# Performance work log

Measured on AMD Instinct MI355X. Metric: run time of the kernel, lower is better.

Reference implementation:

```python
import jax, jax.numpy as jnp
import numpy as np

B, N_HIS, GRAPH_DIM, EMB, N_PRE = 32, 12, 307, 32, 12
DAY_STAMPS, WEEK_STATES = 288, 7
HID = EMB * N_PRE  # 384
STD, MEAN = 50.0, 60.0
LN_EPS = 1e-3  # keras LayerNormalization default epsilon


def setup_inputs() -> dict:
    key = jax.random.key(0)
    ks = jax.random.split(key, 32)
    gn = lambda k, shape, s: (jax.random.normal(k, shape, jnp.float32) * s)
    # inputs: [B, 1+n_his, 2+graph_dim]; row 0 carries (week, date) ids, rows 1: carry data
    x_data = gn(ks[0], (B, N_HIS, GRAPH_DIM), 1.0)
    week = jax.random.randint(ks[1], (B,), 0, WEEK_STATES)
    date = jax.random.randint(ks[2], (B,), 0, DAY_STAMPS)
    inputs = jnp.zeros((B, 1 + N_HIS, 2 + GRAPH_DIM), jnp.float32)
    inputs = inputs.at[:, 0, 0].set(week.astype(jnp.float32))
    inputs = inputs.at[:, 0, 1].set(date.astype(jnp.float32))
    inputs = inputs.at[:, 1:, 2:].set(x_data)
    d = {
        'inputs': inputs,
        'conv_w': gn(ks[3], (EMB,), 0.5),        # 1x1 Conv2D on 1 input channel
        'conv_b': gn(ks[4], (EMB,), 0.1),
        'dws': gn(ks[5], (DAY_STAMPS, N_HIS, EMB, EMB, N_HIS), (2.0 / (EMB * N_HIS)) ** 0.5),
        'dbs': gn(ks[6], (DAY_STAMPS, GRAPH_DIM, EMB, N_HIS), 0.02),
        'ln_gamma': jnp.ones((N_HIS,), jnp.float32),
        'ln_beta': jnp.zeros((N_HIS,), jnp.float32),
        'tge2tg': gn(ks[7], (GRAPH_DIM, EMB, GRAPH_DIM), (1.0 / (GRAPH_DIM * EMB)) ** 0.5),
        'gte2gt': gn(ks[8], (N_HIS, EMB, N_HIS), (1.0 / (N_HIS * EMB)) ** 0.5),
        'fully_w': gn(ks[9], (2 * N_HIS, N_PRE), (1.0 / (2 * N_HIS)) ** 0.5),
    }
    shapes = [(N_HIS, HID), (HID,), (HID, HID), (HID,), (HID, HID), (HID,), (HID, N_PRE), (N_PRE,)]
    names = ['w0', 'b0', 'w1', 'b1', 'w2', 'b2', 'w3', 'b3']
    ki = 10
    for pre in ('se_', 'te_'):
        for nm, sh in zip(names, shapes):
            s = 0.0 if nm.startswith('b') else (2.0 / sum(sh)) ** 0.5
            d[pre + nm] = gn(ks[ki], sh, s) if s > 0 else jnp.zeros(sh, jnp.float32)
            ki += 1
    return d


def _mlp(x, w0, b0, w1, b1, w2, b2, w3, b3):
    # MLP(layer_num=2): Dense(relu) -> Dense -> Dense(relu) -> Dense
    x = jax.nn.relu(x @ w0 + b0) @ w1 + b1
    x = jax.nn.relu(x @ w2 + b2) @ w3 + b3
    return x


def _forward(inputs, conv_w, conv_b, dws, dbs, ln_gamma, ln_beta,
             se_p, te_p, tge2tg, gte2gt, fully_w, date):
    x3 = inputs[:, 1:, 2:]                         # [B, t, g]
    xe = x3[..., None] * conv_w + conv_b           # 1x1 conv -> [B, t, g, e]
    xe = jnp.transpose(xe, (0, 2, 3, 1))           # [B, g, e, t]  ('bget')
    # talinear (dilation=False, week_flag=True): gather per-date weights, batched einsum
    dw = dws[date]                                 # [B, t, e, e, t']  ('bteij')
    db = dbs[date]                                 # [B, g, e, t']
    x = jnp.einsum('bget,bteij->bgij', xe, dw) + db
    # LayerNorm over last axis (n_his), keras default eps=1e-3
    m = jnp.mean(x, axis=-1, keepdims=True)
    v = jnp.var(x, axis=-1, keepdims=True)
    x = (x - m) * jax.lax.rsqrt(v + LN_EPS) * ln_gamma + ln_beta
    x = jnp.where(x >= 0, x, 0.3 * x)              # LeakyReLU(alpha=0.3); dropout inactive at inference
    xe2 = jnp.transpose(x, (0, 3, 1, 2))           # [B, t, g, e]
    tge = xe2
    gte = xe2.reshape(xe2.shape[0], GRAPH_DIM, N_HIS, EMB)  # faithful raw reshape (not transpose)
    x3t = jnp.transpose(x3, (0, 2, 1))             # [B, g, t]
    x1 = _mlp(x3t, *se_p)                          # [B, g, n_pre]
    x2 = _mlp(x3t, *te_p)
    tg = jnp.einsum('gev,btge->btv', tge2tg, tge)  # [B, t, g]
    tg2gt = jnp.transpose(tg, (0, 2, 1))           # [B, g, t]
    gt1 = (tg2gt + x1) * jax.nn.sigmoid(tg2gt)
    gt = jnp.einsum('teo,bgte->bgo', gte2gt, gte)  # [B, g, t]
    gt2 = (gt + x2) * jax.nn.sigmoid(gt)
    out = jnp.concatenate([gt1, gt2], axis=-1) @ fully_w  # [B, g, n_pre]
    out = jnp.transpose(out, (0, 2, 1)) * STD + MEAN      # z_inverse
    return out


def reference(inputs, conv_w, conv_b, dws, dbs, ln_gamma, ln_beta,
              se_w0, se_b0, se_w1, se_b1, se_w2, se_b2, se_w3, se_b3,
              te_w0, te_b0, te_w1, te_b1, te_w2, te_b2, te_w3, te_b3,
              tge2tg, gte2gt, fully_w):
    date = inputs[:, 0, 1].astype(jnp.int32)
    se_p = (se_w0, se_b0, se_w1, se_b1, se_w2, se_b2, se_w3, se_b3)
    te_p = (te_w0, te_b0, te_w1, te_b1, te_w2, te_b2, te_w3, te_b3)
    return _forward(inputs, conv_w, conv_b, dws, dbs, ln_gamma, ln_beta,
                    se_p, te_p, tge2tg, gte2gt, fully_w, date)
```

## Files before the change

### kernel.cpp

```cpp
#include <hip/hip_runtime.h>
#include <hip/hip_bf16.h>

#define NB   32
#define GDIM 307
#define IN_ROW 309
#define IN_B  (13*309)
#define NROWS (NB*GDIM)
#define MPAD  9856

typedef __attribute__((ext_vector_type(8))) short bf16x8;
typedef __attribute__((ext_vector_type(4))) float f32x4;

__device__ __forceinline__ void async_copy16(const void* g, void* l) {
  __builtin_amdgcn_global_load_lds(
      (const __attribute__((address_space(1))) void*)g,
      (__attribute__((address_space(3))) void*)l, 16, 0, 0);
}

__device__ __forceinline__ void mgemm_body(
    const __hip_bfloat16* __restrict__ A, int ldA,
    const __hip_bfloat16* __restrict__ Bt, int ldB,
    const float* bias, void* C, int ldC, long Czoff,
    int M, int N, int kt0, int kt1, int act, int outbf,
    char* smem, int m0, int n0) {
  const int tid = threadIdx.x;
  const int w = tid >> 6, lane = tid & 63;
  f32x4 acc[4][2];
  #pragma unroll
  for (int i=0;i<4;i++)
    #pragma unroll
    for (int j=0;j<2;j++) acc[i][j] = (f32x4){0.f,0.f,0.f,0.f};
  const int wm = (w>>1)*64, wn = (w&1)*32;
  const int l15 = lane & 15, lhi = lane >> 4;

  for (int kt = kt0; kt < kt1; ++kt) {
    const int k0 = kt*64;
    #pragma unroll
    for (int i=0;i<4;i++) {
      int c = w*256 + i*64 + lane;
      int row = c >> 3, j = c & 7;
      int jg = j ^ (row & 7);
      async_copy16(A + (size_t)(m0+row)*ldA + k0 + jg*8, smem + (w*256 + i*64)*16);
    }
    #pragma unroll
    for (int i=0;i<2;i++) {
      int c = w*128 + i*64 + lane;
      int row = c >> 3, j = c & 7;
      int jg = j ^ (row & 7);
      async_copy16(Bt + (size_t)(n0+row)*ldB + k0 + jg*8, smem + 16384 + (w*128 + i*64)*16);
    }
    __syncthreads();
    #pragma unroll
    for (int kk=0;kk<2;kk++) {
      bf16x8 af[4], bfr[2];
      #pragma unroll
      for (int fi=0; fi<4; fi++) {
        int row = wm + fi*16 + l15;
        af[fi] = *(const bf16x8*)(smem + row*128 + (((kk<<2)+lhi) ^ (row&7))*16);
      }
      #pragma unroll
      for (int fj=0; fj<2; fj++) {
        int n = wn + fj*16 + l15;
        bfr[fj] = *(const bf16x8*)(smem + 16384 + n*128 + (((kk<<2)+lhi) ^ (n&7))*16);
      }
      #pragma unroll
      for (int fi=0;fi<4;fi++)
        #pragma unroll
        for (int fj=0;fj<2;fj++)
          acc[fi][fj] = __builtin_amdgcn_mfma_f32_16x16x32_bf16(af[fi], bfr[fj], acc[fi][fj], 0, 0, 0);
    }
    __syncthreads();
  }

  #pragma unroll
  for (int fi=0;fi<4;fi++) {
    int row0 = m0 + wm + fi*16 + lhi*4;
    #pragma unroll
    for (int fj=0;fj<2;fj++) {
      int col = n0 + wn + fj*16 + l15;
      if (col < N) {
        float bv = bias ? bias[col] : 0.f;
        #pragma unroll
        for (int r=0;r<4;r++) {
          int row = row0 + r;
          if (row < M) {
            float v = acc[fi][fj][r] + bv;
            if (act) v = fmaxf(v, 0.f);
            if (outbf)
              ((__hip_bfloat16*)C)[(size_t)row*ldC + col] = __float2bfloat16(v);
            else
              ((float*)C + Czoff)[(size_t)row*ldC + col] = v;
          }
        }
      }
    }
  }
}

__device__ __forceinline__ void tr_tile(const float* src, __hip_bfloat16* dst,
    int sK, int sN, int dR, int ldD, int bx, int by, char* smem, int tid) {
  float (*t)[65] = (float(*)[65])smem;
  int k0 = bx*64, n0 = by*64;
  int tx = tid & 63, ty = tid >> 6;
  for (int r = ty; r < 64; r += 4) {
    int k = k0 + r, n = n0 + tx;
    t[r][tx] = (k < sK && n < sN) ? src[(size_t)k*sN + n] : 0.f;
  }
  __syncthreads();
  for (int r = ty; r < 64; r += 4) {
    int n = n0 + r, k = k0 + tx;
    if (n < dR && k < ldD) dst[(size_t)n*ldD + k] = __float2bfloat16(t[tx][r]);
  }
}

__global__ __launch_bounds__(256) void k_f1(
    const float* __restrict__ inp, const float* __restrict__ dws,
    const float* __restrict__ cw, const float* __restrict__ cb,
    float* __restrict__ A_pre, float* __restrict__ Cp,
    const float* se1, const float* te1,
    __hip_bfloat16* Wse1, __hip_bfloat16* Wte1,
    const float* se0, const float* seb0, const float* te0, const float* teb0,
    __hip_bfloat16* __restrict__ hA_se, __hip_bfloat16* __restrict__ hA_te) {
  __shared__ alignas(16) char smem[23040];
  int bid = blockIdx.x, tid = threadIdx.x;
  if (bid < 384) {
    int b = bid / 12, t = bid - b*12;
    float* scw = (float*)smem;
    float* scb = scw + 32;
    if (tid < 32) { scw[tid] = cw[tid]; scb[tid] = cb[tid]; }
    __syncthreads();
    int date = (int)inp[b*IN_B + 1];
    const float* dw = dws + (size_t)date * 147456 + t*12288;
    for (int r = tid; r < 384; r += 256) {
      float sA = 0.f, sC = 0.f;
      #pragma unroll
      for (int e = 0; e < 32; e++) {
        float v = dw[e*384 + r];
        sA += scw[e] * v;
        sC += scb[e] * v;
      }
      A_pre[(b*12 + t)*384 + r] = sA;
      Cp[(b*12 + t)*384 + r]    = sC;
    }
  } else if (bid < 692) {
    int idx = bid - 384;
    int z = idx / 154, mt = idx - z*154;
    int r0 = mt*64;
    const float* w0 = z ? te0 : se0;
    const float* b0 = z ? teb0 : seb0;
    __hip_bfloat16* H = z ? hA_te : hA_se;
    float* sw = (float*)smem;
    float* sb = sw + 4608;
    float* sx = sb + 384;
    for (int i = tid; i < 4608; i += 256) sw[i] = w0[i];
    for (int i = tid; i < 384; i += 256) sb[i] = b0[i];
    for (int v = tid; v < 768; v += 256) {
      int r = v / 12, t = v - r*12;
      int row = r0 + r;
      float xv = 0.f;
      if (row < NROWS) {
        int b = row / GDIM, g = row - b*GDIM;
        xv = inp[b*IN_B + (1+t)*IN_ROW + 2 + g];
      }
      sx[v] = xv;
    }
    __syncthreads();
    for (int c = tid; c < 384; c += 256) {
      float wv[12];
      #pragma unroll
      for (int t = 0; t < 12; t++) wv[t] = sw[t*384 + c];
      float bv = sb[c];
      for (int r = 0; r < 64; r++) {
        int row = r0 + r;
        if (row >= NROWS) break;
        float acc = bv;
        #pragma unroll
        for (int t = 0; t < 12; t++) acc += sx[r*12+t] * wv[t];
        H[(size_t)row*384 + c] = __float2bfloat16(fmaxf(acc, 0.f));
      }
    }
  } else {
    int s = bid - 692;
    int q = s / 36, u = s % 36;
    tr_tile(q ? te1 : se1, q ? Wte1 : Wse1, 384, 384, 384, 384, u % 6, u / 6, smem, tid);
  }
}

__global__ __launch_bounds__(256) void k_f2(
    const __hip_bfloat16* __restrict__ hA_se, const __hip_bfloat16* __restrict__ hA_te,
    const __hip_bfloat16* __restrict__ Wse1, const __hip_bfloat16* __restrict__ Wte1,
    const float* __restrict__ seb1, const float* __restrict__ teb1,
    __hip_bfloat16* __restrict__ hB_se, __hip_bfloat16* __restrict__ hB_te,
    const float* __restrict__ inp, const float* __restrict__ dbs,
    const float* __restrict__ A_pre, const float* __restrict__ Cp,
    const float* __restrict__ gamma, const float* __restrict__ beta,
    __hip_bfloat16* __restrict__ xlnT, __hip_bfloat16* __restrict__ xg,
    const float* se2, const float* te2, const float* se3, const float* te3,
    const float* g2g, const float* tgw,
    __hip_bfloat16* Wse2, __hip_bfloat16* Wte2, __hip_bfloat16* Wse3,
    __hip_bfloat16* Wte3, __hip_bfloat16* Wgt, __hip_bfloat16* Wtg) {
  __shared__ alignas(16) char smem[32640];
  int bid = blockIdx.x, tid = threadIdx.x;
  if (bid < 924) {
    int z = bid / 462, rem = bid - z*462;
    mgemm_body(z ? hA_te : hA_se, 384, z ? Wte1 : Wse1, 384,
               z ? teb1 : seb1, z ? hB_te : hB_se, 384, 0,
               NROWS, 384, 0, 6, 0, 1, smem, (rem/6)*128, (rem%6)*64);
  } else if (bid < 1784) {
    int s = bid - 924;
    if (s < 770) {
      tr_tile(tgw, Wtg, 9824, 307, 320, 9856, s % 154, s / 154, smem, tid);
    } else if (s < 842) {
      int q = (s-770) / 36, u = (s-770) % 36;
      tr_tile(q ? te2 : se2, q ? Wte2 : Wse2, 384, 384, 384, 384, u % 6, u / 6, smem, tid);
    } else {
      int q = (s-842) / 6, u = (s-842) % 6;
      const float* src = q==0?se3 : q==1?te3 : g2g;
      __hip_bfloat16* dst = q==0?Wse3 : q==1?Wte3 : Wgt;
      tr_tile(src, dst, 384, 12, 64, 384, u, 0, smem, tid);
    }
  } else {
    int idx = bid - 1784;
    int b = idx / 39, gc = idx - b*39;
    int g0 = gc*8, ng = min(8, GDIM - g0);
    float* sA  = (float*)smem;
    float* sxb = sA + 4608;
    float* sCs = sxb + 3072;
    float* sx3 = sCs + 384;
    int date = (int)inp[b*IN_B + 1];
    for (int v = tid; v < 4608; v += 256) sA[v] = A_pre[b*4608 + v];
    for (int e = tid; e < 384; e += 256) {
      float s = 0.f;
      #pragma unroll
      for (int t = 0; t < 12; t++) s += Cp[b*4608 + t*384 + e];
      sCs[e] = s;
    }
    if (tid < ng*12) {
      int gl = tid / 12, t = tid - gl*12;
      sx3[tid] = inp[b*IN_B + (1+t)*IN_ROW + 2 + g0 + gl];
    }
    if (gc == 38) {
      for (int v = tid; v < 384; v += 256) {
        int j = v >> 5, c = v & 31;
        xlnT[(size_t)(b*12+j)*9856 + 9824 + c] = __float2bfloat16(0.f);
      }
    }
    __syncthreads();
    for (int o = tid; o < ng*384; o += 256) {
      int gl = o / 384, e = o - gl*384;
      float acc = sCs[e] + dbs[(size_t)date*117888 + (g0+gl)*384 + e];
      #pragma unroll
      for (int t = 0; t < 12; t++) acc += sx3[gl*12+t] * sA[t*384 + e];
      sxb[gl*384 + e] = acc;
    }
    __syncthreads();
    if (tid < ng*32) {
      int gl = tid >> 5, i = tid & 31;
      const float* xb = sxb + gl*384 + i*12;
      float m = 0.f;
      #pragma unroll
      for (int q = 0; q < 12; q++) m += xb[q];
      m *= (1.f/12.f);
      float v = 0.f;
      #pragma unroll
      for (int q = 0; q < 12; q++) { float d = xb[q] - m; v += d*d; }
      v *= (1.f/12.f);
      float rs = rsqrtf(v + 1e-3f);
      int g = g0 + gl;
      #pragma unroll
      for (int j = 0; j < 12; j++) {
        float y = (xb[j] - m) * rs * gamma[j] + beta[j];
        y = (y >= 0.f) ? y : 0.3f*y;
        __hip_bfloat16 yb = __float2bfloat16(y);
        xlnT[(size_t)(b*12 + j)*9856 + g*32 + i] = yb;
        int q2 = j*GDIM + g;
        int gq = q2 / 12, tq = q2 - gq*12;
        xg[(size_t)(b*GDIM + gq)*384 + tq*32 + i] = yb;
      }
    }
  }
}

__global__ __launch_bounds__(256) void k_f3(
    const __hip_bfloat16* __restrict__ hB_se, const __hip_bfloat16* __restrict__ hB_te,
    const __hip_bfloat16* __restrict__ Wse2, const __hip_bfloat16* __restrict__ Wte2,
    const float* __restrict__ seb2, const float* __restrict__ teb2,
    __hip_bfloat16* __restrict__ hA_se, __hip_bfloat16* __restrict__ hA_te,
    const __hip_bfloat16* __restrict__ xlnT, const __hip_bfloat16* __restrict__ Wtg,
    float* __restrict__ tgp,
    const __hip_bfloat16* __restrict__ xg, const __hip_bfloat16* __restrict__ Wgt,
    float* __restrict__ gtv) {
  __shared__ alignas(16) char smem[24576];
  int bid = blockIdx.x;
  if (bid < 924) {
    int z = bid / 462, rem = bid - z*462;
    mgemm_body(z ? hB_te : hB_se, 384, z ? Wte2 : Wse2, 384,
               z ? teb2 : seb2, z ? hA_te : hA_se, 384, 0,
               NROWS, 384, 0, 6, 1, 1, smem, (rem/6)*128, (rem%6)*64);
  } else if (bid < 1164) {
    int idx = bid - 924;
    int z = idx / 15, rem = idx - z*15;
    int n0 = (rem % 5)*64, m0 = (rem / 5)*128;
    int kt0 = z*10, kt1 = min(154, kt0 + 10);
    mgemm_body(xlnT, 9856, Wtg, 9856, nullptr, tgp, 320, (long)z*122880,
               384, 320, kt0, kt1, 0, 0, smem, m0, n0);
  } else {
    int m0 = (bid - 1164)*128;
    mgemm_body(xg, 384, Wgt, 384, nullptr, gtv, 12, 0,
               NROWS, 12, 0, 6, 0, 0, smem, m0, 0);
  }
}

__global__ __launch_bounds__(256) void k_f4(
    const __hip_bfloat16* __restrict__ hA_se, const __hip_bfloat16* __restrict__ hA_te,
    const __hip_bfloat16* __restrict__ Wse3, const __hip_bfloat16* __restrict__ Wte3,
    const float* __restrict__ seb3, const float* __restrict__ teb3,
    float* __restrict__ x1, float* __restrict__ x2,
    const float* __restrict__ tgp, float* __restrict__ tgv) {
  __shared__ alignas(16) char smem[24576];
  int bid = blockIdx.x;
  if (bid < 154) {
    int z = bid / 77, m0 = (bid - z*77)*128;
    mgemm_body(z ? hA_te : hA_se, 384, z ? Wte3 : Wse3, 384,
               z ? teb3 : seb3, z ? x2 : x1, 12, 0,
               NROWS, 12, 0, 6, 0, 0, smem, m0, 0);
  } else {
    int base = (bid - 154) * 1024;
    #pragma unroll
    for (int q = 0; q < 4; q++) {
      int gid = base + q*256 + threadIdx.x;
      float s = 0.f;
      #pragma unroll
      for (int z = 0; z < 16; z++) s += tgp[(size_t)z*122880 + gid];
      tgv[gid] = s;
    }
  }
}

__global__ __launch_bounds__(256) void k_final(const float* __restrict__ tgv,
    const float* __restrict__ gt, const float* __restrict__ x1,
    const float* __restrict__ x2, const float* __restrict__ fw,
    float* __restrict__ out) {
  __shared__ float w[288];
  for (int idx = threadIdx.x; idx < 288; idx += 256) w[idx] = fw[idx];
  __syncthreads();
  int gid = blockIdx.x*256 + threadIdx.x;
  if (gid >= NROWS) return;
  int b = gid / GDIM, g = gid - b*GDIM;
  float g1[12], g2[12];
  #pragma unroll
  for (int n = 0; n < 12; n++) {
    float tv  = tgv[(size_t)(b*12+n)*320 + g];
    float x1v = x1[(size_t)gid*12 + n];
    float gv  = gt[(size_t)gid*12 + n];
    float x2v = x2[(size_t)gid*12 + n];
    float s1 = 1.f/(1.f + __expf(-tv));
    float s2 = 1.f/(1.f + __expf(-gv));
    g1[n] = (tv + x1v)*s1;
    g2[n] = (gv + x2v)*s2;
  }
  #pragma unroll
  for (int o = 0; o < 12; o++) {
    float acc = 0.f;
    #pragma unroll
    for (int n = 0; n < 12; n++)
      acc += g1[n]*w[n*12+o] + g2[n]*w[(12+n)*12+o];
    out[(size_t)(b*12+o)*GDIM + g] = acc*50.f + 60.f;
  }
}

extern "C" void kernel_launch(void* const* d_in, const int* in_sizes, int n_in,
                              void* d_out, int out_size, void* d_ws, size_t ws_size,
                              hipStream_t stream) {
  const float* inp    = (const float*)d_in[0];
  const float* cw     = (const float*)d_in[1];
  const float* cb     = (const float*)d_in[2];
  const float* dws    = (const float*)d_in[3];
  const float* dbs    = (const float*)d_in[4];
  const float* ln_g   = (const float*)d_in[5];
  const float* ln_b   = (const float*)d_in[6];
  const float* tge2tg = (const float*)d_in[7];
  const float* gte2gt = (const float*)d_in[8];
  const float* fullyw = (const float*)d_in[9];
  const float* se[8];
  const float* te[8];
  for (int i = 0; i < 8; i++) { se[i] = (const float*)d_in[10+i]; te[i] = (const float*)d_in[18+i]; }
  float* out = (float*)d_out;

  char* base = (char*)d_ws;
  size_t off = 0;
  auto alloc = [&](size_t bytes) { char* r = base + off; off += (bytes + 255) & ~(size_t)255; return r; };
  float* A_pre = (float*)alloc(147456*4);
  float* Cp    = (float*)alloc(147456*4);
  float* x1    = (float*)alloc(117888*4);
  float* x2    = (float*)alloc(117888*4);
  float* gtv   = (float*)alloc(117888*4);
  float* tgv   = (float*)alloc(122880*4);
  float* tgp   = (float*)alloc((size_t)16*122880*4);
  __hip_bfloat16* hA_se = (__hip_bfloat16*)alloc((size_t)MPAD*384*2);
  __hip_bfloat16* hA_te = (__hip_bfloat16*)alloc((size_t)MPAD*384*2);
  __hip_bfloat16* hB_se = (__hip_bfloat16*)alloc((size_t)MPAD*384*2);
  __hip_bfloat16* hB_te = (__hip_bfloat16*)alloc((size_t)MPAD*384*2);
  __hip_bfloat16* xlnT  = (__hip_bfloat16*)alloc((size_t)384*9856*2);
  __hip_bfloat16* xg    = (__hip_bfloat16*)alloc((size_t)MPAD*384*2);
  __hip_bfloat16* Wse1 = (__hip_bfloat16*)alloc(147456*2);
  __hip_bfloat16* Wse2 = (__hip_bfloat16*)alloc(147456*2);
  __hip_bfloat16* Wte1 = (__hip_bfloat16*)alloc(147456*2);
  __hip_bfloat16* Wte2 = (__hip_bfloat16*)alloc(147456*2);
  __hip_bfloat16* Wse3 = (__hip_bfloat16*)alloc(24576*2);
  __hip_bfloat16* Wte3 = (__hip_bfloat16*)alloc(24576*2);
  __hip_bfloat16* Wgt  = (__hip_bfloat16*)alloc(24576*2);
  __hip_bfloat16* Wtg  = (__hip_bfloat16*)alloc((size_t)320*9856*2);

  k_f1<<<764, 256, 0, stream>>>(inp, dws, cw, cb, A_pre, Cp,
      se[2], te[2], Wse1, Wte1,
      se[0], se[1], te[0], te[1], hA_se, hA_te);

  k_f2<<<3032, 256, 0, stream>>>(hA_se, hA_te, Wse1, Wte1, se[3], te[3],
      hB_se, hB_te, inp, dbs, A_pre, Cp, ln_g, ln_b, xlnT, xg,
      se[4], te[4], se[6], te[6], gte2gt, tge2tg,
      Wse2, Wte2, Wse3, Wte3, Wgt, Wtg);

  k_f3<<<1241, 256, 0, stream>>>(hB_se, hB_te, Wse2, Wte2, se[5], te[5],
      hA_se, hA_te, xlnT, Wtg, tgp, xg, Wgt, gtv);

  k_f4<<<274, 256, 0, stream>>>(hA_se, hA_te, Wse3, Wte3, se[7], te[7], x1, x2, tgp, tgv);

  k_final<<<39, 256, 0, stream>>>(tgv, gtv, x1, x2, fullyw, out);
}
```

Measured before the change: 109.3 us.

## Fuse final MLP layer, split-K reduction and gating epilogue into one kernel

Merges the last MLP GEMMs (se and te), the 16-way split-K sum of the tg partials, and the sigmoid gating plus fully-connected output into a single kernel. The GEMM results stay in LDS, so x1, x2 and tgv never go through global memory, and one launch is removed. The cost is fewer blocks (77 instead of 274+39), two serial GEMMs per block, and the split-K reduction now done by only 128 threads per block with strided loads.

```diff
diff --git a/kernel.cpp b/kernel.cpp
--- a/kernel.cpp
+++ b/kernel.cpp
@@ -22,7 +22,7 @@
     const __hip_bfloat16* __restrict__ Bt, int ldB,
     const float* bias, void* C, int ldC, long Czoff,
     int M, int N, int kt0, int kt1, int act, int outbf,
-    char* smem, int m0, int n0) {
+    char* smem, int m0, int n0, float* ldsOut) {
   const int tid = threadIdx.x;
   const int w = tid >> 6, lane = tid & 63;
   f32x4 acc[4][2];
@@ -72,6 +72,22 @@
     __syncthreads();
   }
 
+  if (outbf == 2) {
+    #pragma unroll
+    for (int fi=0;fi<4;fi++) {
+      int rl0 = wm + fi*16 + lhi*4;
+      #pragma unroll
+      for (int fj=0;fj<2;fj++) {
+        int col = wn + fj*16 + l15;
+        if (col < N) {
+          float bv = bias ? bias[col] : 0.f;
+          #pragma unroll
+          for (int r=0;r<4;r++) ldsOut[(rl0+r)*13 + col] = acc[fi][fj][r] + bv;
+        }
+      }
+    }
+    return;
+  }
   #pragma unroll
   for (int fi=0;fi<4;fi++) {
     int row0 = m0 + wm + fi*16 + lhi*4;
@@ -205,7 +221,7 @@
     int z = bid / 462, rem = bid - z*462;
     mgemm_body(z ? hA_te : hA_se, 384, z ? Wte1 : Wse1, 384,
                z ? teb1 : seb1, z ? hB_te : hB_se, 384, 0,
-               NROWS, 384, 0, 6, 0, 1, smem, (rem/6)*128, (rem%6)*64);
+               NROWS, 384, 0, 6, 0, 1, smem, (rem/6)*128, (rem%6)*64, nullptr);
   } else if (bid < 1784) {
     int s = bid - 924;
     if (s < 770) {
@@ -296,18 +312,18 @@
     int z = bid / 462, rem = bid - z*462;
     mgemm_body(z ? hB_te : hB_se, 384, z ? Wte2 : Wse2, 384,
                z ? teb2 : seb2, z ? hA_te : hA_se, 384, 0,
-               NROWS, 384, 0, 6, 1, 1, smem, (rem/6)*128, (rem%6)*64);
+               NROWS, 384, 0, 6, 1, 1, smem, (rem/6)*128, (rem%6)*64, nullptr);
   } else if (bid < 1164) {
     int idx = bid - 924;
     int z = idx / 15, rem = idx - z*15;
     int n0 = (rem % 5)*64, m0 = (rem / 5)*128;
     int kt0 = z*10, kt1 = min(154, kt0 + 10);
     mgemm_body(xlnT, 9856, Wtg, 9856, nullptr, tgp, 320, (long)z*122880,
-               384, 320, kt0, kt1, 0, 0, smem, m0, n0);
+               384, 320, kt0, kt1, 0, 0, smem, m0, n0, nullptr);
   } else {
     int m0 = (bid - 1164)*128;
     mgemm_body(xg, 384, Wgt, 384, nullptr, gtv, 12, 0,
-               NROWS, 12, 0, 6, 0, 0, smem, m0, 0);
+               NROWS, 12, 0, 6, 0, 0, smem, m0, 0, nullptr);
   }
 }
 
@@ -315,57 +331,45 @@
     const __hip_bfloat16* __restrict__ hA_se, const __hip_bfloat16* __restrict__ hA_te,
     const __hip_bfloat16* __restrict__ Wse3, const __hip_bfloat16* __restrict__ Wte3,
     const float* __restrict__ seb3, const float* __restrict__ teb3,
-    float* __restrict__ x1, float* __restrict__ x2,
-    const float* __restrict__ tgp, float* __restrict__ tgv) {
+    const float* __restrict__ tgp, const float* __restrict__ gtv,
+    const float* __restrict__ fw, float* __restrict__ out) {
   __shared__ alignas(16) char smem[24576];
-  int bid = blockIdx.x;
-  if (bid < 154) {
-    int z = bid / 77, m0 = (bid - z*77)*128;
-    mgemm_body(z ? hA_te : hA_se, 384, z ? Wte3 : Wse3, 384,
-               z ? teb3 : seb3, z ? x2 : x1, 12, 0,
-               NROWS, 12, 0, 6, 0, 0, smem, m0, 0);
-  } else {
-    int base = (bid - 154) * 1024;
-    #pragma unroll
-    for (int q = 0; q < 4; q++) {
-      int gid = base + q*256 + threadIdx.x;
-      float s = 0.f;
-      #pragma unroll
-      for (int z = 0; z < 16; z++) s += tgp[(size_t)z*122880 + gid];
-      tgv[gid] = s;
-    }
-  }
-}
-
-__global__ __launch_bounds__(256) void k_final(const float* __restrict__ tgv,
-    const float* __restrict__ gt, const float* __restrict__ x1,
-    const float* __restrict__ x2, const float* __restrict__ fw,
-    float* __restrict__ out) {
-  __shared__ float w[288];
-  for (int idx = threadIdx.x; idx < 288; idx += 256) w[idx] = fw[idx];
+  __shared__ float x1s[128*13];
+  __shared__ float x2s[128*13];
+  __shared__ float fws[288];
+  int tid = threadIdx.x;
+  int m0 = blockIdx.x * 128;
+  for (int i = tid; i < 288; i += 256) fws[i] = fw[i];
+  mgemm_body(hA_se, 384, Wse3, 384, seb3, nullptr, 0, 0,
+             NROWS, 12, 0, 6, 0, 2, smem, m0, 0, x1s);
+  mgemm_body(hA_te, 384, Wte3, 384, teb3, nullptr, 0, 0,
+             NROWS, 12, 0, 6, 0, 2, smem, m0, 0, x2s);
   __syncthreads();
-  int gid = blockIdx.x*256 + threadIdx.x;
-  if (gid >= NROWS) return;
-  int b = gid / GDIM, g = gid - b*GDIM;
-  float g1[12], g2[12];
-  #pragma unroll
-  for (int n = 0; n < 12; n++) {
-    float tv  = tgv[(size_t)(b*12+n)*320 + g];
-    float x1v = x1[(size_t)gid*12 + n];
-    float gv  = gt[(size_t)gid*12 + n];
-    float x2v = x2[(size_t)gid*12 + n];
-    float s1 = 1.f/(1.f + __expf(-tv));
-    float s2 = 1.f/(1.f + __expf(-gv));
-    g1[n] = (tv + x1v)*s1;
-    g2[n] = (gv + x2v)*s2;
-  }
-  #pragma unroll
-  for (int o = 0; o < 12; o++) {
-    float acc = 0.f;
-    #pragma unroll
-    for (int n = 0; n < 12; n++)
-      acc += g1[n]*w[n*12+o] + g2[n]*w[(12+n)*12+o];
-    out[(size_t)(b*12+o)*GDIM + g] = acc*50.f + 60.f;
+  if (tid < 128) {
+    int row = m0 + tid;
+    if (row < NROWS) {
+      int b = row / GDIM, g = row - b*GDIM;
+      float g1[12], g2[12];
+      #pragma unroll
+      for (int n = 0; n < 12; n++) {
+        float tv = 0.f;
+        #pragma unroll
+        for (int z = 0; z < 16; z++) tv += tgp[(size_t)z*122880 + (b*12+n)*320 + g];
+        float gv = gtv[(size_t)row*12 + n];
+        float s1 = 1.f/(1.f + __expf(-tv));
+        float s2 = 1.f/(1.f + __expf(-gv));
+        g1[n] = (tv + x1s[tid*13 + n])*s1;
+        g2[n] = (gv + x2s[tid*13 + n])*s2;
+      }
+      #pragma unroll
+      for (int o = 0; o < 12; o++) {
+        float a = 0.f;
+        #pragma unroll
+        for (int n = 0; n < 12; n++)
+          a += g1[n]*fws[n*12+o] + g2[n]*fws[(12+n)*12+o];
+        out[(size_t)(b*12+o)*GDIM + g] = a*50.f + 60.f;
+      }
+    }
   }
 }
 
@@ -392,10 +396,7 @@
   auto alloc = [&](size_t bytes) { char* r = base + off; off += (bytes + 255) & ~(size_t)255; return r; };
   float* A_pre = (float*)alloc(147456*4);
   float* Cp    = (float*)alloc(147456*4);
-  float* x1    = (float*)alloc(117888*4);
-  float* x2    = (float*)alloc(117888*4);
   float* gtv   = (float*)alloc(117888*4);
-  float* tgv   = (float*)alloc(122880*4);
   float* tgp   = (float*)alloc((size_t)16*122880*4);
   __hip_bfloat16* hA_se = (__hip_bfloat16*)alloc((size_t)MPAD*384*2);
   __hip_bfloat16* hA_te = (__hip_bfloat16*)alloc((size_t)MPAD*384*2);
@@ -424,7 +425,6 @@
   k_f3<<<1241, 256, 0, stream>>>(hB_se, hB_te, Wse2, Wte2, se[5], te[5],
       hA_se, hA_te, xlnT, Wtg, tgp, xg, Wgt, gtv);
 
-  k_f4<<<274, 256, 0, stream>>>(hA_se, hA_te, Wse3, Wte3, se[7], te[7], x1, x2, tgp, tgv);
-
-  k_final<<<39, 256, 0, stream>>>(tgv, gtv, x1, x2, fullyw, out);
-}
+  k_f4<<<77, 256, 0, stream>>>(hA_se, hA_te, Wse3, Wte3, se[7], te[7],
+      tgp, gtv, fullyw, out);
+}
```

New measurement: 153.6 us. +40.5%, slower.
